# Optimization experiments

Measured on AMD Instinct MI355X. Metric: run time of the kernel, lower is better.

Reference implementation:

```python
import jax, jax.numpy as jnp
import numpy as np

D_MODEL = 1024
NUM_HEADS = 16
D_K = D_MODEL // NUM_HEADS


def setup_inputs() -> dict:
    key = jax.random.key(0)
    ks = jax.random.split(key, 11)
    B, S, D = 2, 2048, D_MODEL
    s = 1.0 / np.sqrt(D)
    return {
        "query": jax.random.normal(ks[0], (B, S, D), jnp.float32),
        "key": jax.random.normal(ks[1], (B, S, D), jnp.float32),
        "value": jax.random.normal(ks[2], (B, S, D), jnp.float32),
        "Wq": jax.random.normal(ks[3], (D, D), jnp.float32) * s,
        "bq": jnp.zeros((D,), jnp.float32),
        "Wk": jax.random.normal(ks[4], (D, D), jnp.float32) * s,
        "bk": jnp.zeros((D,), jnp.float32),
        "Wv": jax.random.normal(ks[5], (D, D), jnp.float32) * s,
        "bv": jnp.zeros((D,), jnp.float32),
        "Wo": jax.random.normal(ks[6], (D, D), jnp.float32) * s,
        "bo": jnp.zeros((D,), jnp.float32),
    }


def reference(query, key, value, Wq, bq, Wk, bk, Wv, bv, Wo, bo):
    B, S, D = query.shape
    H, Dk = NUM_HEADS, D_K
    # projections, then split heads: [B, H, S, Dk]
    q = (query @ Wq + bq).reshape(B, S, H, Dk).transpose(0, 2, 1, 3)
    k = (key @ Wk + bk).reshape(B, S, H, Dk).transpose(0, 2, 1, 3)
    v = (value @ Wv + bv).reshape(B, S, H, Dk).transpose(0, 2, 1, 3)
    scores = jnp.einsum('bhqd,bhkd->bhqk', q, k) / jnp.sqrt(jnp.float32(Dk))
    attn = jax.nn.softmax(scores, axis=-1)
    out = jnp.einsum('bhqk,bhkd->bhqd', attn, v)  # [B, H, S, Dk]
    out = out.transpose(0, 2, 1, 3).reshape(B, S, D)
    return out @ Wo + bo
```

## Files before the change

### kernel.cpp

```cpp
#include <hip/hip_runtime.h>

typedef unsigned short u16;
typedef unsigned int   u32;
typedef __bf16 bf16x8 __attribute__((ext_vector_type(8)));
typedef float  f32x4  __attribute__((ext_vector_type(4)));

union U16B { int4 i4; bf16x8 b8; u16 u[8]; };
union U16Q { uint2 d2; u16 u[4]; };
union PK4  { uint2 d2; __bf16 b[4]; };

static __device__ __forceinline__ u16 f2b(float f) {
  u32 x = __float_as_uint(f);
  x += 0x7FFFu + ((x >> 16) & 1u);
  return (u16)(x >> 16);
}
static __device__ __forceinline__ float b2f(u16 s) {
  return __uint_as_float(((u32)s) << 16);
}

#define GLOAD_LDS16(g, l) \
  __builtin_amdgcn_global_load_lds((const __attribute__((address_space(1))) u32*)(g), \
                                   (__attribute__((address_space(3))) u32*)(l), 16, 0, 0)

struct ConvA { const float* src[3]; u16* dst[3]; };

__global__ __launch_bounds__(256) void convA(ConvA a) {
  const float* s = a.src[blockIdx.z];
  u16*         d = a.dst[blockIdx.z];
  const size_t i = ((size_t)blockIdx.x * 256 + threadIdx.x) * 8;
  float4 f0 = *(const float4*)(s + i);
  float4 f1 = *(const float4*)(s + i + 4);
  U16B t;
  t.u[0] = f2b(f0.x); t.u[1] = f2b(f0.y); t.u[2] = f2b(f0.z); t.u[3] = f2b(f0.w);
  t.u[4] = f2b(f1.x); t.u[5] = f2b(f1.y); t.u[6] = f2b(f1.z); t.u[7] = f2b(f1.w);
  *(int4*)(d + i) = t.i4;
}

struct TransA { const float* W[4]; u16* Wt[4]; };

__global__ __launch_bounds__(256) void transW(TransA a) {
  const float* W  = a.W[blockIdx.z];
  u16*         Wt = a.Wt[blockIdx.z];
  __shared__ float t[64][65];
  const int bx = blockIdx.x * 64, by = blockIdx.y * 64;
  const int tx = threadIdx.x & 63, ty = threadIdx.x >> 6;
  #pragma unroll
  for (int j = 0; j < 16; ++j) {
    int row = j * 4 + ty;
    t[row][tx] = W[(size_t)(by + row) * 1024 + bx + tx];
  }
  __syncthreads();
  #pragma unroll
  for (int j = 0; j < 16; ++j) {
    int row = j * 4 + ty;
    Wt[(size_t)(bx + row) * 1024 + by + tx] = f2b(t[tx][row]);
  }
}

struct GemmB { const u16* A[3]; const u16* Bt[3]; const float* bias[3]; void* C[3]; int mode[3]; int cpx; };

__global__ __launch_bounds__(256) void gemm_bt(GemmB g) {
  constexpr int K = 1024, N = 1024;
  __shared__ u16 As[128 * 64];
  __shared__ u16 Bs[128 * 64];
  const int bid = blockIdx.x;
  const int lg = (bid & 7) * g.cpx + (bid >> 3);
  const int z = lg >> 8;
  const int rem = lg & 255;
  const int row0 = (rem >> 3) * 128, col0 = (rem & 7) * 128;
  const u16*   Ap   = g.A[z];
  const u16*   Bt   = g.Bt[z];
  const float* bias = g.bias[z];
  const int mode = g.mode[z];
  const int tid = threadIdx.x;
  const int wid = tid >> 6, lane = tid & 63;
  const int wr = wid >> 1, wc = wid & 1;
  const int lo = lane & 15, hi = lane >> 4;
  const int rs = tid >> 3, us = tid & 7;
  const int sw = (us ^ (rs & 7)) * 8;

  f32x4 acc[4][4];
  const f32x4 z4 = {0.f, 0.f, 0.f, 0.f};
  #pragma unroll
  for (int i = 0; i < 4; ++i)
    #pragma unroll
    for (int j = 0; j < 4; ++j) acc[i][j] = z4;

  for (int kt = 0; kt < K / 64; ++kt) {
    __syncthreads();
    #pragma unroll
    for (int c = 0; c < 4; ++c) {
      int r = c * 32 + rs;
      GLOAD_LDS16(Ap + (size_t)(row0 + r) * K + kt * 64 + sw, &As[r * 64 + us * 8]);
      GLOAD_LDS16(Bt + (size_t)(col0 + r) * K + kt * 64 + sw, &Bs[r * 64 + us * 8]);
    }
    __syncthreads();
    #pragma unroll
    for (int ks = 0; ks < 2; ++ks) {
      bf16x8 af[4], bfr[4];
      #pragma unroll
      for (int mf = 0; mf < 4; ++mf) {
        int r = wr * 64 + mf * 16 + lo;
        af[mf] = *(const bf16x8*)&As[r * 64 + (((ks * 4 + hi) ^ (r & 7)) << 3)];
      }
      #pragma unroll
      for (int nf = 0; nf < 4; ++nf) {
        int r = wc * 64 + nf * 16 + lo;
        bfr[nf] = *(const bf16x8*)&Bs[r * 64 + (((ks * 4 + hi) ^ (r & 7)) << 3)];
      }
      #pragma unroll
      for (int mf = 0; mf < 4; ++mf)
        #pragma unroll
        for (int nf = 0; nf < 4; ++nf)
          acc[mf][nf] = __builtin_amdgcn_mfma_f32_16x16x32_bf16(af[mf], bfr[nf], acc[mf][nf], 0, 0, 0);
    }
  }

  #pragma unroll
  for (int nf = 0; nf < 4; ++nf) {
    int col = col0 + wc * 64 + nf * 16 + lo;
    float bv = bias[col];
    #pragma unroll
    for (int mf = 0; mf < 4; ++mf) {
      int rb = row0 + wr * 64 + mf * 16 + hi * 4;
      if (mode == 2) {
        U16Q q4;
        #pragma unroll
        for (int e = 0; e < 4; ++e) q4.u[e] = f2b(acc[mf][nf][e] + bv);
        *(uint2*)&((u16*)g.C[z])[(size_t)col * 4096 + rb] = q4.d2;
      } else {
        #pragma unroll
        for (int e = 0; e < 4; ++e) {
          float v = acc[mf][nf][e] + bv;
          if (mode == 1) ((float*)g.C[z])[(size_t)(rb + e) * N + col] = v;
          else           ((u16*)g.C[z])[(size_t)(rb + e) * N + col] = f2b(v);
        }
      }
    }
  }
}

__global__ __launch_bounds__(256) void attn_fwd(const u16* __restrict__ Q,
                                                const u16* __restrict__ Kp,
                                                const u16* __restrict__ VpT,
                                                u16* __restrict__ O) {
  __shared__ u16 Ks[64 * 64];
  __shared__ u16 Vts[64 * 64];
  __shared__ u16 Ps[64 * 64];
  const int tid = threadIdx.x;
  const int bid = blockIdx.x;
  const int t = bid >> 3;
  const int hb = (bid & 7) * 4 + (t >> 5);
  const int qb = t & 31;
  const int h = hb & 15, b = hb >> 4;
  const int wid = tid >> 6, lane = tid & 63;
  const int lo = lane & 15, hi = lane >> 4;
  const int rs = tid >> 3, us = tid & 7;
  const int hoff = h * 64;
  const size_t rowQ0 = (size_t)b * 2048 + (size_t)qb * 64;
  const float QSCALE = 0.125f * 1.4426950408889634f;

  bf16x8 qf[2];
  #pragma unroll
  for (int ks = 0; ks < 2; ++ks) {
    size_t r = rowQ0 + wid * 16 + lo;
    U16B in; in.i4 = *(const int4*)&Q[r * 1024 + hoff + ks * 32 + hi * 8];
    U16B o;
    #pragma unroll
    for (int j = 0; j < 8; ++j) o.u[j] = f2b(b2f(in.u[j]) * QSCALE);
    qf[ks] = o.b8;
  }

  f32x4 oacc[4];
  const f32x4 z4 = {0.f, 0.f, 0.f, 0.f};
  #pragma unroll
  for (int df = 0; df < 4; ++df) oacc[df] = z4;
  float m_r = -1e30f, l_r = 0.f;

  for (int kb = 0; kb < 32; ++kb) {
    const int kv0 = kb * 64;
    __syncthreads();
    #pragma unroll
    for (int c = 0; c < 2; ++c) {
      int r = c * 32 + rs;
      int lds = r * 64 + ((us ^ (r & 7)) << 3);
      *(int4*)&Ks[lds]  = *(const int4*)&Kp[((size_t)b * 2048 + kv0 + r) * 1024 + hoff + us * 8];
      *(int4*)&Vts[lds] = *(const int4*)&VpT[(size_t)(hoff + r) * 4096 + b * 2048 + kv0 + us * 8];
    }
    __syncthreads();

    f32x4 sfr[4];
    #pragma unroll
    for (int nf = 0; nf < 4; ++nf) sfr[nf] = z4;
    #pragma unroll
    for (int ks = 0; ks < 2; ++ks) {
      #pragma unroll
      for (int nf = 0; nf < 4; ++nf) {
        int kk = nf * 16 + lo;
        bf16x8 kf = *(const bf16x8*)&Ks[kk * 64 + (((ks * 4 + hi) ^ (kk & 7)) << 3)];
        sfr[nf] = __builtin_amdgcn_mfma_f32_16x16x32_bf16(kf, qf[ks], sfr[nf], 0, 0, 0);
      }
    }

    float pm = -1e30f;
    #pragma unroll
    for (int nf = 0; nf < 4; ++nf)
      #pragma unroll
      for (int e = 0; e < 4; ++e) pm = fmaxf(pm, sfr[nf][e]);
    pm = fmaxf(pm, __shfl_xor(pm, 16));
    pm = fmaxf(pm, __shfl_xor(pm, 32));
    float mn = fmaxf(m_r, pm);
    float cc = __builtin_amdgcn_exp2f(m_r - mn);
    m_r = mn;
    float ps = 0.f;
    #pragma unroll
    for (int nf = 0; nf < 4; ++nf) {
      PK4 pk;
      #pragma unroll
      for (int e = 0; e < 4; ++e) {
        float p = __builtin_amdgcn_exp2f(sfr[nf][e] - mn);
        ps += p;
        pk.b[e] = (__bf16)p;
      }
      *(uint2*)&Ps[(wid * 16 + lo) * 64 + ((nf * 16 + hi * 4) ^ ((lo & 7) << 3))] = pk.d2;
    }
    ps += __shfl_xor(ps, 16);
    ps += __shfl_xor(ps, 32);
    l_r = l_r * cc + ps;
    float cce[4];
    #pragma unroll
    for (int e = 0; e < 4; ++e) cce[e] = __shfl(cc, hi * 4 + e);
    __syncthreads();

    #pragma unroll
    for (int ksp = 0; ksp < 2; ++ksp) {
      bf16x8 pa = *(const bf16x8*)&Ps[(wid * 16 + lo) * 64 + ((((ksp * 4 + hi) ^ (lo & 7))) << 3)];
      bf16x8 vb[4];
      #pragma unroll
      for (int df = 0; df < 4; ++df) {
        int d = df * 16 + lo;
        vb[df] = *(const bf16x8*)&Vts[d * 64 + (((ksp * 4 + hi) ^ (d & 7)) << 3)];
      }
      if (ksp == 0) {
        #pragma unroll
        for (int df = 0; df < 4; ++df)
          #pragma unroll
          for (int e = 0; e < 4; ++e) oacc[df][e] *= cce[e];
      }
      #pragma unroll
      for (int df = 0; df < 4; ++df)
        oacc[df] = __builtin_amdgcn_mfma_f32_16x16x32_bf16(pa, vb[df], oacc[df], 0, 0, 0);
    }
  }

  float inv = __builtin_amdgcn_rcpf(l_r);
  float inve[4];
  #pragma unroll
  for (int e = 0; e < 4; ++e) inve[e] = __shfl(inv, hi * 4 + e);
  #pragma unroll
  for (int df = 0; df < 4; ++df)
    #pragma unroll
    for (int e = 0; e < 4; ++e) {
      size_t row = rowQ0 + wid * 16 + hi * 4 + e;
      O[row * 1024 + hoff + df * 16 + lo] = f2b(oacc[df][e] * inve[e]);
    }
}

extern "C" void kernel_launch(void* const* d_in, const int* in_sizes, int n_in,
                              void* d_out, int out_size, void* d_ws, size_t ws_size,
                              hipStream_t stream) {
  (void)in_sizes; (void)n_in; (void)out_size;
  const size_t MB = 1024 * 1024;
  if (ws_size < 40 * MB) return;
  char* ws = (char*)d_ws;
  u16* Wqt = (u16*)(ws + 0 * MB);
  u16* Wkt = (u16*)(ws + 2 * MB);
  u16* Wvt = (u16*)(ws + 4 * MB);
  u16* Wot = (u16*)(ws + 6 * MB);
  u16* Vb  = (u16*)(ws + 8 * MB);
  u16* Qp  = (u16*)(ws + 16 * MB);
  u16* Kp  = (u16*)(ws + 24 * MB);
  u16* VpT = (u16*)(ws + 32 * MB);
  u16* Op  = (u16*)(ws + 8 * MB);
  u16* Qb = (u16*)d_out;
  u16* Kb = (u16*)d_out + (size_t)4 * MB;

  ConvA ca;
  ca.src[0] = (const float*)d_in[0]; ca.dst[0] = Qb;
  ca.src[1] = (const float*)d_in[1]; ca.dst[1] = Kb;
  ca.src[2] = (const float*)d_in[2]; ca.dst[2] = Vb;
  hipLaunchKernelGGL(convA, dim3(2048, 1, 3), dim3(256), 0, stream, ca);

  TransA ta;
  ta.W[0] = (const float*)d_in[3]; ta.Wt[0] = Wqt;
  ta.W[1] = (const float*)d_in[5]; ta.Wt[1] = Wkt;
  ta.W[2] = (const float*)d_in[7]; ta.Wt[2] = Wvt;
  ta.W[3] = (const float*)d_in[9]; ta.Wt[3] = Wot;
  hipLaunchKernelGGL(transW, dim3(16, 16, 4), dim3(256), 0, stream, ta);

  GemmB gp;
  gp.A[0] = Qb; gp.Bt[0] = Wqt; gp.bias[0] = (const float*)d_in[4]; gp.C[0] = Qp;  gp.mode[0] = 0;
  gp.A[1] = Kb; gp.Bt[1] = Wkt; gp.bias[1] = (const float*)d_in[6]; gp.C[1] = Kp;  gp.mode[1] = 0;
  gp.A[2] = Vb; gp.Bt[2] = Wvt; gp.bias[2] = (const float*)d_in[8]; gp.C[2] = VpT; gp.mode[2] = 2;
  gp.cpx = 96;
  hipLaunchKernelGGL(gemm_bt, dim3(768), dim3(256), 0, stream, gp);

  hipLaunchKernelGGL(attn_fwd, dim3(1024), dim3(256), 0, stream, Qp, Kp, VpT, Op);

  GemmB gf;
  gf.A[0] = Op; gf.Bt[0] = Wot; gf.bias[0] = (const float*)d_in[10]; gf.C[0] = (void*)d_out; gf.mode[0] = 1;
  gf.A[1] = nullptr; gf.A[2] = nullptr; gf.Bt[1] = nullptr; gf.Bt[2] = nullptr;
  gf.bias[1] = nullptr; gf.bias[2] = nullptr; gf.C[1] = nullptr; gf.C[2] = nullptr;
  gf.mode[1] = 0; gf.mode[2] = 0;
  gf.cpx = 32;
  hipLaunchKernelGGL(gemm_bt, dim3(256), dim3(256), 0, stream, gf);
}
```

Baseline: 159.6 us.

## Double-buffer K/V tiles with async global-to-LDS loads in attention

Attention now keeps two LDS buffers for the K and V tiles. It prefetches the next tile with global_load_lds direct-to-LDS loads while the current tile is computed, and moves the XOR swizzle from the LDS address to the global address. This removes the register round-trip on K/V loads and lets memory latency overlap with the MFMA and softmax work. The barrier after writing P is also dropped, since each wave reads back only its own rows. In exchange the kernel uses twice the LDS for K/V, which may lower occupancy, and it relies on the top-of-loop barrier to wait for the async loads.

```diff
diff --git a/kernel.cpp b/kernel.cpp
--- a/kernel.cpp
+++ b/kernel.cpp
@@ -144,8 +144,8 @@
                                                 const u16* __restrict__ Kp,
                                                 const u16* __restrict__ VpT,
                                                 u16* __restrict__ O) {
-  __shared__ u16 Ks[64 * 64];
-  __shared__ u16 Vts[64 * 64];
+  __shared__ u16 Ks[2][64 * 64];
+  __shared__ u16 Vts[2][64 * 64];
   __shared__ u16 Ps[64 * 64];
   const int tid = threadIdx.x;
   const int bid = blockIdx.x;
@@ -177,17 +177,29 @@
   for (int df = 0; df < 4; ++df) oacc[df] = z4;
   float m_r = -1e30f, l_r = 0.f;
 
+  #pragma unroll
+  for (int c = 0; c < 2; ++c) {
+    int r = c * 32 + rs;
+    int swu = (us ^ (r & 7)) * 8;
+    GLOAD_LDS16(&Kp[((size_t)b * 2048 + r) * 1024 + hoff + swu], &Ks[0][r * 64 + us * 8]);
+    GLOAD_LDS16(&VpT[(size_t)(hoff + r) * 4096 + b * 2048 + swu], &Vts[0][r * 64 + us * 8]);
+  }
+
   for (int kb = 0; kb < 32; ++kb) {
-    const int kv0 = kb * 64;
+    const int cur = kb & 1;
     __syncthreads();
-    #pragma unroll
-    for (int c = 0; c < 2; ++c) {
-      int r = c * 32 + rs;
-      int lds = r * 64 + ((us ^ (r & 7)) << 3);
-      *(int4*)&Ks[lds]  = *(const int4*)&Kp[((size_t)b * 2048 + kv0 + r) * 1024 + hoff + us * 8];
-      *(int4*)&Vts[lds] = *(const int4*)&VpT[(size_t)(hoff + r) * 4096 + b * 2048 + kv0 + us * 8];
-    }
-    __syncthreads();
+    if (kb < 31) {
+      const int kv0 = (kb + 1) * 64;
+      #pragma unroll
+      for (int c = 0; c < 2; ++c) {
+        int r = c * 32 + rs;
+        int swu = (us ^ (r & 7)) * 8;
+        GLOAD_LDS16(&Kp[((size_t)b * 2048 + kv0 + r) * 1024 + hoff + swu],
+                    &Ks[cur ^ 1][r * 64 + us * 8]);
+        GLOAD_LDS16(&VpT[(size_t)(hoff + r) * 4096 + b * 2048 + kv0 + swu],
+                    &Vts[cur ^ 1][r * 64 + us * 8]);
+      }
+    }
 
     f32x4 sfr[4];
     #pragma unroll
@@ -197,7 +209,7 @@
       #pragma unroll
       for (int nf = 0; nf < 4; ++nf) {
         int kk = nf * 16 + lo;
-        bf16x8 kf = *(const bf16x8*)&Ks[kk * 64 + (((ks * 4 + hi) ^ (kk & 7)) << 3)];
+        bf16x8 kf = *(const bf16x8*)&Ks[cur][kk * 64 + (((ks * 4 + hi) ^ (kk & 7)) << 3)];
         sfr[nf] = __builtin_amdgcn_mfma_f32_16x16x32_bf16(kf, qf[ks], sfr[nf], 0, 0, 0);
       }
     }
@@ -230,7 +242,6 @@
     float cce[4];
     #pragma unroll
     for (int e = 0; e < 4; ++e) cce[e] = __shfl(cc, hi * 4 + e);
-    __syncthreads();
 
     #pragma unroll
     for (int ksp = 0; ksp < 2; ++ksp) {
@@ -239,7 +250,7 @@
       #pragma unroll
       for (int df = 0; df < 4; ++df) {
         int d = df * 16 + lo;
-        vb[df] = *(const bf16x8*)&Vts[d * 64 + (((ksp * 4 + hi) ^ (d & 7)) << 3)];
+        vb[df] = *(const bf16x8*)&Vts[cur][d * 64 + (((ksp * 4 + hi) ^ (d & 7)) << 3)];
       }
       if (ksp == 0) {
         #pragma unroll
```

Result: no change. 159.0 us (-0.4%).

## Split attention over two KV halves, add combine kernel, use direct-to-LDS loads

Applied to the files above, without the earlier changes.

The attention kernel now splits each query tile's key/value range into two halves, doubling the grid to 2048 blocks. Each block writes unnormalized partial outputs plus per-row max and sum. A new combine kernel rescales and merges the two partials into the final bf16 output. The K/V tile loads now use global_load_lds with the swizzle moved to the source address, and the barrier between the P store and the P·V MFMAs is removed. The aim is better CU occupancy and fewer stalls, at the cost of an extra launch and extra partial-output traffic through the scratch buffer.

```diff
diff --git a/kernel.cpp b/kernel.cpp
--- a/kernel.cpp
+++ b/kernel.cpp
@@ -143,15 +143,17 @@
 __global__ __launch_bounds__(256) void attn_fwd(const u16* __restrict__ Q,
                                                 const u16* __restrict__ Kp,
                                                 const u16* __restrict__ VpT,
-                                                u16* __restrict__ O) {
+                                                u16* __restrict__ Part,
+                                                float2* __restrict__ St) {
   __shared__ u16 Ks[64 * 64];
   __shared__ u16 Vts[64 * 64];
   __shared__ u16 Ps[64 * 64];
   const int tid = threadIdx.x;
   const int bid = blockIdx.x;
   const int t = bid >> 3;
-  const int hb = (bid & 7) * 4 + (t >> 5);
-  const int qb = t & 31;
+  const int hb = (bid & 7) * 4 + (t >> 6);
+  const int qb = (t & 63) >> 1;
+  const int split = t & 1;
   const int h = hb & 15, b = hb >> 4;
   const int wid = tid >> 6, lane = tid & 63;
   const int lo = lane & 15, hi = lane >> 4;
@@ -159,6 +161,7 @@
   const int hoff = h * 64;
   const size_t rowQ0 = (size_t)b * 2048 + (size_t)qb * 64;
   const float QSCALE = 0.125f * 1.4426950408889634f;
+  const int kb0 = split * 16;
 
   bf16x8 qf[2];
   #pragma unroll
@@ -177,15 +180,15 @@
   for (int df = 0; df < 4; ++df) oacc[df] = z4;
   float m_r = -1e30f, l_r = 0.f;
 
-  for (int kb = 0; kb < 32; ++kb) {
-    const int kv0 = kb * 64;
+  for (int kb = 0; kb < 16; ++kb) {
+    const int kv0 = (kb0 + kb) * 64;
     __syncthreads();
     #pragma unroll
     for (int c = 0; c < 2; ++c) {
       int r = c * 32 + rs;
-      int lds = r * 64 + ((us ^ (r & 7)) << 3);
-      *(int4*)&Ks[lds]  = *(const int4*)&Kp[((size_t)b * 2048 + kv0 + r) * 1024 + hoff + us * 8];
-      *(int4*)&Vts[lds] = *(const int4*)&VpT[(size_t)(hoff + r) * 4096 + b * 2048 + kv0 + us * 8];
+      int swu = (us ^ (r & 7)) * 8;
+      GLOAD_LDS16(&Kp[((size_t)b * 2048 + kv0 + r) * 1024 + hoff + swu], &Ks[r * 64 + us * 8]);
+      GLOAD_LDS16(&VpT[(size_t)(hoff + r) * 4096 + b * 2048 + kv0 + swu], &Vts[r * 64 + us * 8]);
     }
     __syncthreads();
 
@@ -230,7 +233,6 @@
     float cce[4];
     #pragma unroll
     for (int e = 0; e < 4; ++e) cce[e] = __shfl(cc, hi * 4 + e);
-    __syncthreads();
 
     #pragma unroll
     for (int ksp = 0; ksp < 2; ++ksp) {
@@ -253,17 +255,42 @@
     }
   }
 
-  float inv = __builtin_amdgcn_rcpf(l_r);
-  float inve[4];
-  #pragma unroll
-  for (int e = 0; e < 4; ++e) inve[e] = __shfl(inv, hi * 4 + e);
+  u16* Po = Part + (size_t)split * 4096 * 1024;
   #pragma unroll
   for (int df = 0; df < 4; ++df)
     #pragma unroll
     for (int e = 0; e < 4; ++e) {
       size_t row = rowQ0 + wid * 16 + hi * 4 + e;
-      O[row * 1024 + hoff + df * 16 + lo] = f2b(oacc[df][e] * inve[e]);
-    }
+      Po[row * 1024 + hoff + df * 16 + lo] = f2b(oacc[df][e]);
+    }
+  if (hi == 0) {
+    size_t qg = (size_t)qb * 64 + wid * 16 + lo;
+    St[((size_t)(split * 2 + b) * 16 + h) * 2048 + qg] = make_float2(m_r, l_r);
+  }
+}
+
+__global__ __launch_bounds__(256) void attn_combine(const u16* __restrict__ Part,
+                                                    const float2* __restrict__ St,
+                                                    u16* __restrict__ Op) {
+  const size_t i = ((size_t)blockIdx.x * 256 + threadIdx.x) * 8;
+  const int row = (int)(i >> 10);
+  const int col = (int)(i & 1023);
+  const int h = col >> 6;
+  const int b = row >> 11, q = row & 2047;
+  const float2 s0 = St[((size_t)(0 + b) * 16 + h) * 2048 + q];
+  const float2 s1 = St[((size_t)(2 + b) * 16 + h) * 2048 + q];
+  const float m = fmaxf(s0.x, s1.x);
+  float w0 = __builtin_amdgcn_exp2f(s0.x - m);
+  float w1 = __builtin_amdgcn_exp2f(s1.x - m);
+  const float inv = __builtin_amdgcn_rcpf(w0 * s0.y + w1 * s1.y);
+  w0 *= inv; w1 *= inv;
+  U16B p0, p1, o;
+  p0.i4 = *(const int4*)(Part + i);
+  p1.i4 = *(const int4*)(Part + (size_t)4096 * 1024 + i);
+  #pragma unroll
+  for (int j = 0; j < 8; ++j)
+    o.u[j] = f2b(w0 * b2f(p0.u[j]) + w1 * b2f(p1.u[j]));
+  *(int4*)(Op + i) = o.i4;
 }
 
 extern "C" void kernel_launch(void* const* d_in, const int* in_sizes, int n_in,
@@ -282,8 +309,10 @@
   u16* Kp  = (u16*)(ws + 24 * MB);
   u16* VpT = (u16*)(ws + 32 * MB);
   u16* Op  = (u16*)(ws + 8 * MB);
+  float2* St = (float2*)(ws + 0 * MB);
   u16* Qb = (u16*)d_out;
   u16* Kb = (u16*)d_out + (size_t)4 * MB;
+  u16* Part = (u16*)d_out;
 
   ConvA ca;
   ca.src[0] = (const float*)d_in[0]; ca.dst[0] = Qb;
@@ -305,7 +334,8 @@
   gp.cpx = 96;
   hipLaunchKernelGGL(gemm_bt, dim3(768), dim3(256), 0, stream, gp);
 
-  hipLaunchKernelGGL(attn_fwd, dim3(1024), dim3(256), 0, stream, Qp, Kp, VpT, Op);
+  hipLaunchKernelGGL(attn_fwd, dim3(2048), dim3(256), 0, stream, Qp, Kp, VpT, Part, St);
+  hipLaunchKernelGGL(attn_combine, dim3(2048), dim3(256), 0, stream, Part, St, Op);
 
   GemmB gf;
   gf.A[0] = Op; gf.Bt[0] = Wot; gf.bias[0] = (const float*)d_in[10]; gf.C[0] = (void*)d_out; gf.mode[0] = 1;
```

Measured after the change: 164.4 us. +3.1%, slower.

## Rewrite attention with 32x32 MFMA, register-resident P, and async K/V loads

Applied to the files above, without the earlier changes.

The attention kernel moves from 16x16x32 to 32x32x16 bf16 MFMA and gives each wave 32 query rows, so a block now covers 128 queries and the grid is halved. The probability tile stays in registers and is rearranged with lane shuffles instead of a round trip through shared memory, which removes a barrier and the P buffer. K/V tiles are loaded with global_load_lds direct-to-LDS using a source-side swizzle. The output is staged through LDS so it can be written as coalesced 16-byte stores. Risks are higher register pressure and fewer blocks to spread across the CUs.

```diff
diff --git a/kernel.cpp b/kernel.cpp
--- a/kernel.cpp
+++ b/kernel.cpp
@@ -4,10 +4,12 @@
 typedef unsigned int   u32;
 typedef __bf16 bf16x8 __attribute__((ext_vector_type(8)));
 typedef float  f32x4  __attribute__((ext_vector_type(4)));
+typedef float  f32x16 __attribute__((ext_vector_type(16)));
 
 union U16B { int4 i4; bf16x8 b8; u16 u[8]; };
 union U16Q { uint2 d2; u16 u[4]; };
-union PK4  { uint2 d2; __bf16 b[4]; };
+union PK2  { u32 w; __bf16 b[2]; };
+union BF8W { u32 w[4]; bf16x8 v; };
 
 static __device__ __forceinline__ u16 f2b(float f) {
   u32 x = __float_as_uint(f);
@@ -16,6 +18,9 @@
 }
 static __device__ __forceinline__ float b2f(u16 s) {
   return __uint_as_float(((u32)s) << 16);
+}
+static __device__ __forceinline__ u32 pk2(float a, float b) {
+  PK2 p; p.b[0] = (__bf16)a; p.b[1] = (__bf16)b; return p.w;
 }
 
 #define GLOAD_LDS16(g, l) \
@@ -144,38 +149,43 @@
                                                 const u16* __restrict__ Kp,
                                                 const u16* __restrict__ VpT,
                                                 u16* __restrict__ O) {
-  __shared__ u16 Ks[64 * 64];
-  __shared__ u16 Vts[64 * 64];
-  __shared__ u16 Ps[64 * 64];
+  __shared__ u16 shm[2 * 64 * 64];
+  u16* Ks  = shm;
+  u16* Vts = shm + 64 * 64;
   const int tid = threadIdx.x;
   const int bid = blockIdx.x;
   const int t = bid >> 3;
-  const int hb = (bid & 7) * 4 + (t >> 5);
-  const int qb = t & 31;
+  const int hb = (bid & 7) * 4 + (t >> 4);
+  const int qb = t & 15;
   const int h = hb & 15, b = hb >> 4;
   const int wid = tid >> 6, lane = tid & 63;
-  const int lo = lane & 15, hi = lane >> 4;
+  const int lq = lane & 31;
+  const int hh = lane >> 5;
   const int rs = tid >> 3, us = tid & 7;
   const int hoff = h * 64;
-  const size_t rowQ0 = (size_t)b * 2048 + (size_t)qb * 64;
+  const size_t rowQ0 = (size_t)b * 2048 + (size_t)qb * 128;
+  const int woff = wid * 32;
   const float QSCALE = 0.125f * 1.4426950408889634f;
 
-  bf16x8 qf[2];
-  #pragma unroll
-  for (int ks = 0; ks < 2; ++ks) {
-    size_t r = rowQ0 + wid * 16 + lo;
-    U16B in; in.i4 = *(const int4*)&Q[r * 1024 + hoff + ks * 32 + hi * 8];
+  bf16x8 qf[4];
+  #pragma unroll
+  for (int ds = 0; ds < 4; ++ds) {
+    size_t r = rowQ0 + woff + lq;
+    U16B in; in.i4 = *(const int4*)&Q[r * 1024 + hoff + ds * 16 + hh * 8];
     U16B o;
     #pragma unroll
     for (int j = 0; j < 8; ++j) o.u[j] = f2b(b2f(in.u[j]) * QSCALE);
-    qf[ks] = o.b8;
-  }
-
-  f32x4 oacc[4];
-  const f32x4 z4 = {0.f, 0.f, 0.f, 0.f};
-  #pragma unroll
-  for (int df = 0; df < 4; ++df) oacc[df] = z4;
+    qf[ds] = o.b8;
+  }
+
+  f32x16 oacc[2];
+  #pragma unroll
+  for (int dt = 0; dt < 2; ++dt)
+    #pragma unroll
+    for (int r = 0; r < 16; ++r) oacc[dt][r] = 0.f;
   float m_r = -1e30f, l_r = 0.f;
+
+  const int swz = lane & 7;
 
   for (int kb = 0; kb < 32; ++kb) {
     const int kv0 = kb * 64;
@@ -183,87 +193,104 @@
     #pragma unroll
     for (int c = 0; c < 2; ++c) {
       int r = c * 32 + rs;
-      int lds = r * 64 + ((us ^ (r & 7)) << 3);
-      *(int4*)&Ks[lds]  = *(const int4*)&Kp[((size_t)b * 2048 + kv0 + r) * 1024 + hoff + us * 8];
-      *(int4*)&Vts[lds] = *(const int4*)&VpT[(size_t)(hoff + r) * 4096 + b * 2048 + kv0 + us * 8];
+      int swu = (us ^ (r & 7)) * 8;
+      GLOAD_LDS16(&Kp[((size_t)b * 2048 + kv0 + r) * 1024 + hoff + swu], &Ks[r * 64 + us * 8]);
+      GLOAD_LDS16(&VpT[(size_t)(hoff + r) * 4096 + b * 2048 + kv0 + swu], &Vts[r * 64 + us * 8]);
     }
     __syncthreads();
 
-    f32x4 sfr[4];
-    #pragma unroll
-    for (int nf = 0; nf < 4; ++nf) sfr[nf] = z4;
-    #pragma unroll
-    for (int ks = 0; ks < 2; ++ks) {
-      #pragma unroll
-      for (int nf = 0; nf < 4; ++nf) {
-        int kk = nf * 16 + lo;
-        bf16x8 kf = *(const bf16x8*)&Ks[kk * 64 + (((ks * 4 + hi) ^ (kk & 7)) << 3)];
-        sfr[nf] = __builtin_amdgcn_mfma_f32_16x16x32_bf16(kf, qf[ks], sfr[nf], 0, 0, 0);
-      }
+    f32x16 s0, s1;
+    #pragma unroll
+    for (int r = 0; r < 16; ++r) { s0[r] = 0.f; s1[r] = 0.f; }
+    #pragma unroll
+    for (int ds = 0; ds < 4; ++ds) {
+      int u = 2 * ds + hh;
+      bf16x8 k0 = *(const bf16x8*)&Ks[lq * 64 + ((u ^ swz) << 3)];
+      bf16x8 k1 = *(const bf16x8*)&Ks[(32 + lq) * 64 + ((u ^ swz) << 3)];
+      s0 = __builtin_amdgcn_mfma_f32_32x32x16_bf16(k0, qf[ds], s0, 0, 0, 0);
+      s1 = __builtin_amdgcn_mfma_f32_32x32x16_bf16(k1, qf[ds], s1, 0, 0, 0);
     }
 
     float pm = -1e30f;
     #pragma unroll
-    for (int nf = 0; nf < 4; ++nf)
-      #pragma unroll
-      for (int e = 0; e < 4; ++e) pm = fmaxf(pm, sfr[nf][e]);
-    pm = fmaxf(pm, __shfl_xor(pm, 16));
+    for (int r = 0; r < 16; ++r) pm = fmaxf(pm, fmaxf(s0[r], s1[r]));
     pm = fmaxf(pm, __shfl_xor(pm, 32));
     float mn = fmaxf(m_r, pm);
     float cc = __builtin_amdgcn_exp2f(m_r - mn);
     m_r = mn;
+    #pragma unroll
+    for (int dt = 0; dt < 2; ++dt)
+      #pragma unroll
+      for (int r = 0; r < 16; ++r) oacc[dt][r] *= cc;
     float ps = 0.f;
-    #pragma unroll
-    for (int nf = 0; nf < 4; ++nf) {
-      PK4 pk;
-      #pragma unroll
-      for (int e = 0; e < 4; ++e) {
-        float p = __builtin_amdgcn_exp2f(sfr[nf][e] - mn);
-        ps += p;
-        pk.b[e] = (__bf16)p;
-      }
-      *(uint2*)&Ps[(wid * 16 + lo) * 64 + ((nf * 16 + hi * 4) ^ ((lo & 7) << 3))] = pk.d2;
-    }
-    ps += __shfl_xor(ps, 16);
+    u32 c[16];
+    #pragma unroll
+    for (int m = 0; m < 8; ++m) {
+      float e0 = __builtin_amdgcn_exp2f(s0[2 * m] - mn);
+      float e1 = __builtin_amdgcn_exp2f(s0[2 * m + 1] - mn);
+      ps += e0 + e1;
+      c[m] = pk2(e0, e1);
+    }
+    #pragma unroll
+    for (int m = 0; m < 8; ++m) {
+      float e0 = __builtin_amdgcn_exp2f(s1[2 * m] - mn);
+      float e1 = __builtin_amdgcn_exp2f(s1[2 * m + 1] - mn);
+      ps += e0 + e1;
+      c[8 + m] = pk2(e0, e1);
+    }
     ps += __shfl_xor(ps, 32);
     l_r = l_r * cc + ps;
-    float cce[4];
-    #pragma unroll
-    for (int e = 0; e < 4; ++e) cce[e] = __shfl(cc, hi * 4 + e);
-    __syncthreads();
-
-    #pragma unroll
-    for (int ksp = 0; ksp < 2; ++ksp) {
-      bf16x8 pa = *(const bf16x8*)&Ps[(wid * 16 + lo) * 64 + ((((ksp * 4 + hi) ^ (lo & 7))) << 3)];
-      bf16x8 vb[4];
-      #pragma unroll
-      for (int df = 0; df < 4; ++df) {
-        int d = df * 16 + lo;
-        vb[df] = *(const bf16x8*)&Vts[d * 64 + (((ksp * 4 + hi) ^ (d & 7)) << 3)];
+
+    u32 x[16];
+    #pragma unroll
+    for (int m = 0; m < 16; ++m) x[m] = (u32)__shfl_xor((int)c[m], 32);
+
+    #pragma unroll
+    for (int sub = 0; sub < 2; ++sub) {
+      const int cb = sub * 8;
+      #pragma unroll
+      for (int ksp = 0; ksp < 2; ++ksp) {
+        BF8W bw;
+        if (ksp == 0) {
+          bw.w[0] = hh ? x[cb + 2] : c[cb + 0];
+          bw.w[1] = hh ? x[cb + 3] : c[cb + 1];
+          bw.w[2] = hh ? c[cb + 2] : x[cb + 0];
+          bw.w[3] = hh ? c[cb + 3] : x[cb + 1];
+        } else {
+          bw.w[0] = hh ? x[cb + 6] : c[cb + 4];
+          bw.w[1] = hh ? x[cb + 7] : c[cb + 5];
+          bw.w[2] = hh ? c[cb + 6] : x[cb + 4];
+          bw.w[3] = hh ? c[cb + 7] : x[cb + 5];
+        }
+        int u = 4 * sub + 2 * ksp + hh;
+        #pragma unroll
+        for (int dt = 0; dt < 2; ++dt) {
+          bf16x8 va = *(const bf16x8*)&Vts[(dt * 32 + lq) * 64 + ((u ^ swz) << 3)];
+          oacc[dt] = __builtin_amdgcn_mfma_f32_32x32x16_bf16(va, bw.v, oacc[dt], 0, 0, 0);
+        }
       }
-      if (ksp == 0) {
-        #pragma unroll
-        for (int df = 0; df < 4; ++df)
-          #pragma unroll
-          for (int e = 0; e < 4; ++e) oacc[df][e] *= cce[e];
-      }
-      #pragma unroll
-      for (int df = 0; df < 4; ++df)
-        oacc[df] = __builtin_amdgcn_mfma_f32_16x16x32_bf16(pa, vb[df], oacc[df], 0, 0, 0);
     }
   }
 
   float inv = __builtin_amdgcn_rcpf(l_r);
-  float inve[4];
-  #pragma unroll
-  for (int e = 0; e < 4; ++e) inve[e] = __shfl(inv, hi * 4 + e);
-  #pragma unroll
-  for (int df = 0; df < 4; ++df)
-    #pragma unroll
-    for (int e = 0; e < 4; ++e) {
-      size_t row = rowQ0 + wid * 16 + hi * 4 + e;
-      O[row * 1024 + hoff + df * 16 + lo] = f2b(oacc[df][e] * inve[e]);
-    }
+  __syncthreads();
+  u16* wreg = shm + wid * 2048;
+  #pragma unroll
+  for (int dt = 0; dt < 2; ++dt)
+    #pragma unroll
+    for (int m = 0; m < 8; ++m) {
+      int bcol = ((2 * m) & 3) + 8 * (m >> 1) + 4 * hh + 32 * dt;
+      u32 pw = pk2(oacc[dt][2 * m] * inv, oacc[dt][2 * m + 1] * inv);
+      char* p = (char*)wreg + lq * 128 + (((bcol >> 3) ^ (lq & 7)) << 4) + (bcol & 7) * 2;
+      *(u32*)p = pw;
+    }
+  #pragma unroll
+  for (int pss = 0; pss < 4; ++pss) {
+    int q = pss * 8 + (lane >> 3);
+    int u = lane & 7;
+    int4 v = *(const int4*)((const char*)wreg + q * 128 + ((u ^ (q & 7)) << 4));
+    *(int4*)&O[(rowQ0 + woff + q) * 1024 + hoff + u * 8] = v;
+  }
 }
 
 extern "C" void kernel_launch(void* const* d_in, const int* in_sizes, int n_in,
@@ -305,7 +332,7 @@
   gp.cpx = 96;
   hipLaunchKernelGGL(gemm_bt, dim3(768), dim3(256), 0, stream, gp);
 
-  hipLaunchKernelGGL(attn_fwd, dim3(1024), dim3(256), 0, stream, Qp, Kp, VpT, Op);
+  hipLaunchKernelGGL(attn_fwd, dim3(512), dim3(256), 0, stream, Qp, Kp, VpT, Op);
 
   GemmB gf;
   gf.A[0] = Op; gf.Bt[0] = Wot; gf.bias[0] = (const float*)d_in[10]; gf.C[0] = (void*)d_out; gf.mode[0] = 1;
```

Result: no change. 162.1 us (+1.6%).
